# Optimization experiments

Hardware: AMD Instinct MI355X
Metric: run time of the kernel (lower is better)

Reference implementation:

```python
import jax, jax.numpy as jnp
import numpy as np

NUM_BINS = 8
TAIL_BOUND = 10.0
MIN_BIN_WIDTH = 1e-3
MIN_BIN_HEIGHT = 1e-3
MIN_DERIVATIVE = 1e-3
N, D = 1048576, 32


def _knots(unnorm, min_size, bound):
    # unnorm: (D, K) -> bin sizes and cumulative knot positions in [-bound, bound]
    K = unnorm.shape[-1]
    sizes = jax.nn.softmax(unnorm, axis=-1)
    sizes = min_size + (1.0 - min_size * K) * sizes
    cum = jnp.concatenate([jnp.zeros((unnorm.shape[0], 1), unnorm.dtype), jnp.cumsum(sizes, axis=-1)], axis=-1)
    cum = 2.0 * bound * cum - bound
    cum = cum.at[:, 0].set(-bound).at[:, -1].set(bound)
    sizes = jnp.diff(cum, axis=-1)
    return sizes, cum


def _bank_log_prob(x, uw, uh, ud):
    # x: (N, D); uw, uh: (D, K); ud: (D, K-1)
    K = uw.shape[-1]
    B = TAIL_BOUND
    # linear tails: pad boundary derivatives so softplus(c)+min_deriv == 1
    c = float(np.log(np.expm1(1.0 - MIN_DERIVATIVE)))
    ud_pad = jnp.pad(ud, ((0, 0), (1, 1)), constant_values=c)            # (D, K+1)
    widths, cumw = _knots(uw, MIN_BIN_WIDTH, B)                           # (D,K),(D,K+1)
    heights, cumh = _knots(uh, MIN_BIN_HEIGHT, B)
    derivs = MIN_DERIVATIVE + jax.nn.softplus(ud_pad)                     # (D, K+1)

    inside = (x >= -B) & (x <= B)
    xc = jnp.clip(x, -B, B)
    # searchsorted per (n, d): bin index in [0, K-1]
    idx = jnp.clip(jnp.sum(xc[..., None] >= cumw[None, :, :], axis=-1) - 1, 0, K - 1)  # (N, D)

    def gather(t, i):
        return jnp.take_along_axis(t[None], i[..., None], axis=-1)[..., 0]

    cw = gather(cumw, idx)
    w = gather(widths, idx)
    ch = gather(cumh, idx)
    h = gather(heights, idx)
    d0 = gather(derivs, idx)
    d1 = gather(derivs, idx + 1)

    delta = h / w
    theta = (xc - cw) / w
    t1m = theta * (1.0 - theta)
    denom = delta + (d0 + d1 - 2.0 * delta) * t1m
    z_in = ch + h * (delta * theta * theta + d0 * t1m) / denom
    logdet_in = jnp.log(delta * delta * (d1 * theta * theta + 2.0 * delta * t1m + d0 * (1.0 - theta) ** 2)) - 2.0 * jnp.log(denom)

    z = jnp.where(inside, z_in, x)            # identity outside [-B, B]
    logdet = jnp.where(inside, logdet_in, 0.0)
    log2pi = float(np.log(2.0 * np.pi))
    return -0.5 * z * z - 0.5 * log2pi + logdet  # (N, D) per-dim log-prob


def setup_inputs() -> dict:
    key = jax.random.key(0)
    kx, kw, kh, kd = jax.random.split(key, 4)
    return {
        "x": 3.0 * jax.random.normal(kx, (N, D), dtype=jnp.float32),
        "unnorm_widths": jax.random.normal(kw, (D, NUM_BINS), dtype=jnp.float32),
        "unnorm_heights": jax.random.normal(kh, (D, NUM_BINS), dtype=jnp.float32),
        "unnorm_derivs": jax.random.normal(kd, (D, NUM_BINS - 1), dtype=jnp.float32),
    }


def reference(x, unnorm_widths, unnorm_heights, unnorm_derivs):
    return _bank_log_prob(x, unnorm_widths, unnorm_heights, unnorm_derivs)
```

## Files before the change

### kernel.cpp

```cpp
#include <hip/hip_runtime.h>
#include <hip/hip_fp16.h>
#include <math.h>

#define NB 8
#define DD 32
constexpr float TB   = 10.0f;
constexpr float MBW  = 1e-3f;
constexpr float MBH  = 1e-3f;
constexpr float MDER = 1e-3f;

__device__ __forceinline__ float softplusf(float v) {
    return (v > 20.0f) ? v : log1pf(expf(v));
}

__global__ __launch_bounds__(256, 4) void mfb_kernel(
    const float* __restrict__ x,
    const float* __restrict__ uw,
    const float* __restrict__ uh,
    const float* __restrict__ ud,
    float* __restrict__ out,
    int n4)
{
    __shared__ float4 s_T[DD][NB + 1];
    __shared__ float  s_kn[DD][7];

    const int t = threadIdx.x;

    if (t < DD) {
        float posw[NB + 1], posh[NB + 1], dv[NB + 1];
        {
            float u[NB];
            float m = -1e30f;
            #pragma unroll
            for (int k = 0; k < NB; ++k) { u[k] = uw[t * NB + k]; m = fmaxf(m, u[k]); }
            float s = 0.0f;
            #pragma unroll
            for (int k = 0; k < NB; ++k) { u[k] = expf(u[k] - m); s += u[k]; }
            const float inv = 1.0f / s;
            posw[0] = -TB;
            float cum = 0.0f;
            #pragma unroll
            for (int k = 0; k < NB; ++k) {
                cum += MBW + (1.0f - MBW * (float)NB) * (u[k] * inv);
                posw[k + 1] = 2.0f * TB * cum - TB;
            }
            posw[NB] = TB;
        }
        {
            float u[NB];
            float m = -1e30f;
            #pragma unroll
            for (int k = 0; k < NB; ++k) { u[k] = uh[t * NB + k]; m = fmaxf(m, u[k]); }
            float s = 0.0f;
            #pragma unroll
            for (int k = 0; k < NB; ++k) { u[k] = expf(u[k] - m); s += u[k]; }
            const float inv = 1.0f / s;
            posh[0] = -TB;
            float cum = 0.0f;
            #pragma unroll
            for (int k = 0; k < NB; ++k) {
                cum += MBH + (1.0f - MBH * (float)NB) * (u[k] * inv);
                posh[k + 1] = 2.0f * TB * cum - TB;
            }
            posh[NB] = TB;
        }
        {
            const float c   = logf(expm1f(1.0f - MDER));
            const float bnd = MDER + softplusf(c);
            dv[0]  = bnd;
            dv[NB] = bnd;
            #pragma unroll
            for (int k = 1; k < NB; ++k)
                dv[k] = MDER + softplusf(ud[t * (NB - 1) + (k - 1)]);
        }
        #pragma unroll
        for (int k = 0; k < 7; ++k) s_kn[t][k] = posw[k + 1];
        const int key = (t >> 2) & 7;
        #pragma unroll
        for (int b = 0; b < NB; ++b) {
            const float w    = posw[b + 1] - posw[b];
            const float invw = 1.0f / w;
            const unsigned u1 = ((unsigned)__half_as_ushort(__float2half_rn(posh[b + 1] - posh[b])) << 16)
                              |  (unsigned)__half_as_ushort(__float2half_rn(posh[b]));
            const unsigned u2 = ((unsigned)__half_as_ushort(__float2half_rn(dv[b + 1])) << 16)
                              |  (unsigned)__half_as_ushort(__float2half_rn(dv[b]));
            float4 T;
            T.x = invw;
            T.y = -posw[b] * invw;
            T.z = __uint_as_float(u1);
            T.w = __uint_as_float(u2);
            s_T[t][b ^ key] = T;
        }
    }
    __syncthreads();

    constexpr float HALF_LOG_2PI = 0.91893853320467274178f;
    constexpr float LN2          = 0.69314718055994530942f;

    const int g      = blockIdx.x * blockDim.x + t;
    const int stride = gridDim.x * blockDim.x;
    const int dbase  = (g * 4) & (DD - 1);
    const int key    = (dbase >> 2) & 7;

    float a0 = s_kn[dbase + 0][0], a1 = s_kn[dbase + 0][1], a2 = s_kn[dbase + 0][2],
          a3 = s_kn[dbase + 0][3], a4 = s_kn[dbase + 0][4], a5 = s_kn[dbase + 0][5],
          a6 = s_kn[dbase + 0][6];
    float b0 = s_kn[dbase + 1][0], b1 = s_kn[dbase + 1][1], b2 = s_kn[dbase + 1][2],
          b3 = s_kn[dbase + 1][3], b4 = s_kn[dbase + 1][4], b5 = s_kn[dbase + 1][5],
          b6 = s_kn[dbase + 1][6];
    float c0 = s_kn[dbase + 2][0], c1 = s_kn[dbase + 2][1], c2 = s_kn[dbase + 2][2],
          c3 = s_kn[dbase + 2][3], c4 = s_kn[dbase + 2][4], c5 = s_kn[dbase + 2][5],
          c6 = s_kn[dbase + 2][6];
    float e0 = s_kn[dbase + 3][0], e1 = s_kn[dbase + 3][1], e2 = s_kn[dbase + 3][2],
          e3 = s_kn[dbase + 3][3], e4 = s_kn[dbase + 3][4], e5 = s_kn[dbase + 3][5],
          e6 = s_kn[dbase + 3][6];

    const float4* __restrict__ r0 = &s_T[dbase + 0][0];
    const float4* __restrict__ r1 = &s_T[dbase + 1][0];
    const float4* __restrict__ r2 = &s_T[dbase + 2][0];
    const float4* __restrict__ r3 = &s_T[dbase + 3][0];

    auto evalone = [&](float xx,
                       float k0, float k1, float k2, float k3, float k4, float k5, float k6,
                       const float4* __restrict__ row) -> float {
        int idx = 0;
        idx += (xx >= k0) ? 1 : 0;
        idx += (xx >= k1) ? 1 : 0;
        idx += (xx >= k2) ? 1 : 0;
        idx += (xx >= k3) ? 1 : 0;
        idx += (xx >= k4) ? 1 : 0;
        idx += (xx >= k5) ? 1 : 0;
        idx += (xx >= k6) ? 1 : 0;

        const float4 T = row[idx ^ key];

        const unsigned u1 = __float_as_uint(T.z);
        const unsigned u2 = __float_as_uint(T.w);
        const float ch = __half2float(__ushort_as_half((unsigned short)(u1 & 0xffffu)));
        const float h  = __half2float(__ushort_as_half((unsigned short)(u1 >> 16)));
        const float d0 = __half2float(__ushort_as_half((unsigned short)(u2 & 0xffffu)));
        const float d1 = __half2float(__ushort_as_half((unsigned short)(u2 >> 16)));

        const float xc    = fminf(fmaxf(xx, -TB), TB);
        const float theta = fmaf(xc, T.x, T.y);
        const float delta = h * T.x;
        const float B     = h * d0;
        const float A     = fmaf(h, delta, -B);
        const float s2    = (d0 + d1) - (delta + delta);
        const float u     = fmaf(-theta, theta, theta);
        const float den   = fmaf(s2, u, delta);
        const float rden  = __builtin_amdgcn_rcpf(den);
        const float num1  = theta * fmaf(theta, A, B);
        const float zin   = fmaf(num1, rden, ch);
        const float dmd   = delta - d0;
        const float poly  = fmaf(fmaf(s2, theta, dmd + dmd), theta, d0);
        const float ee    = delta * rden;
        const float larg  = poly * (ee * ee);
        const float lg2   = __log2f(larg);
        const float z  = (fabsf(xx) <= TB) ? zin : xx;
        const float ld = fmaf(lg2, LN2, -HALF_LOG_2PI);
        return fmaf(z * z, -0.5f, ld);
    };

    const float4* __restrict__ x4 = reinterpret_cast<const float4*>(x);
    float4* __restrict__ o4 = reinterpret_cast<float4*>(out);

    int i = g;
    for (; i + stride < n4; i += 2 * stride) {
        const float4 xa = x4[i];
        const float4 xb = x4[i + stride];
        float4 ra, rb;
        ra.x = evalone(xa.x, a0, a1, a2, a3, a4, a5, a6, r0);
        ra.y = evalone(xa.y, b0, b1, b2, b3, b4, b5, b6, r1);
        ra.z = evalone(xa.z, c0, c1, c2, c3, c4, c5, c6, r2);
        ra.w = evalone(xa.w, e0, e1, e2, e3, e4, e5, e6, r3);
        rb.x = evalone(xb.x, a0, a1, a2, a3, a4, a5, a6, r0);
        rb.y = evalone(xb.y, b0, b1, b2, b3, b4, b5, b6, r1);
        rb.z = evalone(xb.z, c0, c1, c2, c3, c4, c5, c6, r2);
        rb.w = evalone(xb.w, e0, e1, e2, e3, e4, e5, e6, r3);
        o4[i] = ra;
        o4[i + stride] = rb;
    }
    for (; i < n4; i += stride) {
        const float4 xa = x4[i];
        float4 ra;
        ra.x = evalone(xa.x, a0, a1, a2, a3, a4, a5, a6, r0);
        ra.y = evalone(xa.y, b0, b1, b2, b3, b4, b5, b6, r1);
        ra.z = evalone(xa.z, c0, c1, c2, c3, c4, c5, c6, r2);
        ra.w = evalone(xa.w, e0, e1, e2, e3, e4, e5, e6, r3);
        o4[i] = ra;
    }
}

extern "C" void kernel_launch(void* const* d_in, const int* in_sizes, int n_in,
                              void* d_out, int out_size, void* d_ws, size_t ws_size,
                              hipStream_t stream) {
    const float* x  = (const float*)d_in[0];
    const float* uw = (const float*)d_in[1];
    const float* uh = (const float*)d_in[2];
    const float* ud = (const float*)d_in[3];
    float* out = (float*)d_out;

    const int n4 = in_sizes[0] / 4;
    int blocks = (n4 + 255) / 256;
    if (blocks > 2048) blocks = 2048;

    mfb_kernel<<<blocks, 256, 0, stream>>>(x, uw, uh, ud, out, n4);
}
```

Baseline: 59.06 us.

## Unroll grid-stride loop to four loads, use nontemporal stores, raise occupancy

Unrolls the grid-stride loop so each thread issues four float4 loads before computing, and writes results with nontemporal stores to avoid polluting cache with streaming output. It also raises the launch_bounds min-blocks hint from 4 to 8 and rebalances the bin-index comparison sum into a tree. The aim is more memory-level parallelism and less cache traffic on a bandwidth-bound elementwise kernel. The risks are register-pressure spills from the 8-block hint combined with the 4x unroll, and the remainder loop handling more iterations.

After: 160.9 us. 173% more time.

```diff
diff --git a/kernel.cpp b/kernel.cpp
--- a/kernel.cpp
+++ b/kernel.cpp
@@ -9,11 +9,13 @@
 constexpr float MBH  = 1e-3f;
 constexpr float MDER = 1e-3f;
 
+typedef float f32x4 __attribute__((ext_vector_type(4)));
+
 __device__ __forceinline__ float softplusf(float v) {
     return (v > 20.0f) ? v : log1pf(expf(v));
 }
 
-__global__ __launch_bounds__(256, 4) void mfb_kernel(
+__global__ __launch_bounds__(256, 8) void mfb_kernel(
     const float* __restrict__ x,
     const float* __restrict__ uw,
     const float* __restrict__ uh,
@@ -123,14 +125,11 @@
     auto evalone = [&](float xx,
                        float k0, float k1, float k2, float k3, float k4, float k5, float k6,
                        const float4* __restrict__ row) -> float {
-        int idx = 0;
-        idx += (xx >= k0) ? 1 : 0;
-        idx += (xx >= k1) ? 1 : 0;
-        idx += (xx >= k2) ? 1 : 0;
-        idx += (xx >= k3) ? 1 : 0;
-        idx += (xx >= k4) ? 1 : 0;
-        idx += (xx >= k5) ? 1 : 0;
-        idx += (xx >= k6) ? 1 : 0;
+        int i01 = ((xx >= k0) ? 1 : 0) + ((xx >= k1) ? 1 : 0);
+        int i23 = ((xx >= k2) ? 1 : 0) + ((xx >= k3) ? 1 : 0);
+        int i45 = ((xx >= k4) ? 1 : 0) + ((xx >= k5) ? 1 : 0);
+        int i6  = ((xx >= k6) ? 1 : 0);
+        int idx = (i01 + i23) + (i45 + i6);
 
         const float4 T = row[idx ^ key];
 
@@ -162,33 +161,32 @@
         return fmaf(z * z, -0.5f, ld);
     };
 
-    const float4* __restrict__ x4 = reinterpret_cast<const float4*>(x);
-    float4* __restrict__ o4 = reinterpret_cast<float4*>(out);
+    auto eval4 = [&](f32x4 xv) -> f32x4 {
+        f32x4 r;
+        r.x = evalone(xv.x, a0, a1, a2, a3, a4, a5, a6, r0);
+        r.y = evalone(xv.y, b0, b1, b2, b3, b4, b5, b6, r1);
+        r.z = evalone(xv.z, c0, c1, c2, c3, c4, c5, c6, r2);
+        r.w = evalone(xv.w, e0, e1, e2, e3, e4, e5, e6, r3);
+        return r;
+    };
+
+    const f32x4* __restrict__ x4 = reinterpret_cast<const f32x4*>(x);
+    f32x4* __restrict__ o4 = reinterpret_cast<f32x4*>(out);
 
     int i = g;
-    for (; i + stride < n4; i += 2 * stride) {
-        const float4 xa = x4[i];
-        const float4 xb = x4[i + stride];
-        float4 ra, rb;
-        ra.x = evalone(xa.x, a0, a1, a2, a3, a4, a5, a6, r0);
-        ra.y = evalone(xa.y, b0, b1, b2, b3, b4, b5, b6, r1);
-        ra.z = evalone(xa.z, c0, c1, c2, c3, c4, c5, c6, r2);
-        ra.w = evalone(xa.w, e0, e1, e2, e3, e4, e5, e6, r3);
-        rb.x = evalone(xb.x, a0, a1, a2, a3, a4, a5, a6, r0);
-        rb.y = evalone(xb.y, b0, b1, b2, b3, b4, b5, b6, r1);
-        rb.z = evalone(xb.z, c0, c1, c2, c3, c4, c5, c6, r2);
-        rb.w = evalone(xb.w, e0, e1, e2, e3, e4, e5, e6, r3);
-        o4[i] = ra;
-        o4[i + stride] = rb;
+    for (; i + 3 * stride < n4; i += 4 * stride) {
+        const f32x4 xv0 = x4[i];
+        const f32x4 xv1 = x4[i + stride];
+        const f32x4 xv2 = x4[i + 2 * stride];
+        const f32x4 xv3 = x4[i + 3 * stride];
+        __builtin_nontemporal_store(eval4(xv0), &o4[i]);
+        __builtin_nontemporal_store(eval4(xv1), &o4[i + stride]);
+        __builtin_nontemporal_store(eval4(xv2), &o4[i + 2 * stride]);
+        __builtin_nontemporal_store(eval4(xv3), &o4[i + 3 * stride]);
     }
     for (; i < n4; i += stride) {
-        const float4 xa = x4[i];
-        float4 ra;
-        ra.x = evalone(xa.x, a0, a1, a2, a3, a4, a5, a6, r0);
-        ra.y = evalone(xa.y, b0, b1, b2, b3, b4, b5, b6, r1);
-        ra.z = evalone(xa.z, c0, c1, c2, c3, c4, c5, c6, r2);
-        ra.w = evalone(xa.w, e0, e1, e2, e3, e4, e5, e6, r3);
-        o4[i] = ra;
+        const f32x4 xv0 = x4[i];
+        __builtin_nontemporal_store(eval4(xv0), &o4[i]);
     }
 }
 
```
